# Optimization experiments

Hardware: AMD Instinct MI355X
Metric: run time of the kernel (lower is better)

## Reference

```python
import jax, jax.numpy as jnp
import numpy as np

D_MODEL = 1024
NHEAD = 16
D_K = D_MODEL // NHEAD


def setup_inputs() -> dict:
    key = jax.random.key(0)
    ks = jax.random.split(key, 8)
    B, S, D = 4, 2048, D_MODEL
    scale = 1.0 / np.sqrt(D)  # rough xavier-like scale for weights
    return {
        "query": jax.random.normal(ks[0], (B, S, D), jnp.float32),
        "key_": jax.random.normal(ks[1], (B, S, D), jnp.float32),
        "value": jax.random.normal(ks[2], (B, S, D), jnp.float32),
        "w_q": jax.random.normal(ks[3], (D, D), jnp.float32) * scale,
        "w_k": jax.random.normal(ks[4], (D, D), jnp.float32) * scale,
        "w_v": jax.random.normal(ks[5], (D, D), jnp.float32) * scale,
        "w_o": jax.random.normal(ks[6], (D, D), jnp.float32) * scale,
        "b_o": jnp.zeros((D,), jnp.float32),
    }


def reference(query, key_, value, w_q, w_k, w_v, w_o, b_o):
    B, S, D = query.shape
    H, dk = NHEAD, D_K
    # torch Linear: x @ W.T ; reshape to [B, H, S, dk]
    def split_heads(x, w):
        return (x @ w.T).reshape(B, S, H, dk).transpose(0, 2, 1, 3)

    Q = split_heads(query, w_q)
    K = split_heads(key_, w_k)
    V = split_heads(value, w_v)

    scores = jnp.einsum("bhqd,bhkd->bhqk", Q, K) / jnp.sqrt(jnp.float32(dk))
    attn = jax.nn.softmax(scores, axis=-1)  # [B,H,S,S]
    ctx = jnp.einsum("bhqk,bhkd->bhqd", attn, V)
    ctx = ctx.transpose(0, 2, 1, 3).reshape(B, S, D)
    out = ctx @ w_o.T + b_o
    return out
```

## Files before the change

kernel.cpp:

```cpp
#include <hip/hip_runtime.h>
#include <hip/hip_bf16.h>
#include <stdint.h>

#define D_MODEL 1024
#define NHEAD   16
#define DK      64
#define BATCH   4
#define SEQ     2048
#define MROWS   (BATCH*SEQ)

typedef __hip_bfloat16 bf16;
typedef __attribute__((ext_vector_type(8))) short short8;
typedef __attribute__((ext_vector_type(4))) float f32x4;
typedef __attribute__((ext_vector_type(4))) unsigned int uint4t;

typedef __attribute__((address_space(1))) unsigned int as1_uint;
typedef __attribute__((address_space(3))) unsigned int as3_uint;

#define MFMA32(a,b,c) __builtin_amdgcn_mfma_f32_16x16x32_bf16((a),(b),(c),0,0,0)

static __device__ __forceinline__ void load_lds16(const bf16* g, bf16* l) {
  __builtin_amdgcn_global_load_lds((const as1_uint*)g, (as3_uint*)l, 16, 0, 0);
}

static __device__ __forceinline__ unsigned short bfbits(float x) {
  __hip_bfloat16 h = __float2bfloat16(x);
  return __builtin_bit_cast(unsigned short, h);
}

static __device__ __forceinline__ unsigned int pack2(float lo, float hi) {
  return (unsigned int)bfbits(lo) | ((unsigned int)bfbits(hi) << 16);
}

static __device__ __forceinline__ unsigned int pack2t(float lo, float hi) {
  return (__builtin_bit_cast(unsigned int, lo) >> 16) |
         (__builtin_bit_cast(unsigned int, hi) & 0xffff0000u);
}

__global__ __launch_bounds__(256) void cast_w(const float* __restrict__ i0,
                                              const float* __restrict__ i1,
                                              const float* __restrict__ i2,
                                              const float* __restrict__ i3,
                                              bf16* o0, bf16* o1, bf16* o2, bf16* o3,
                                              float s1) {
  const int z = blockIdx.z;
  const float* in = z == 0 ? i0 : (z == 1 ? i1 : (z == 2 ? i2 : i3));
  bf16* out = z == 0 ? o0 : (z == 1 ? o1 : (z == 2 ? o2 : o3));
  const float s = (z == 1) ? s1 : 1.0f;
  int i = blockIdx.x * 256 + threadIdx.x;
  const float4* p = (const float4*)in;
  float4 a = p[2 * (size_t)i];
  float4 b = p[2 * (size_t)i + 1];
  uint4t u;
  u.x = pack2(a.x * s, a.y * s);
  u.y = pack2(a.z * s, a.w * s);
  u.z = pack2(b.x * s, b.y * s);
  u.w = pack2(b.z * s, b.w * s);
  *(uint4t*)(out + (size_t)i * 8) = u;
}

__global__ __launch_bounds__(256) void cast_x(const float* __restrict__ i0,
                                              const float* __restrict__ i1,
                                              const float* __restrict__ i2,
                                              bf16* o0, bf16* o1, bf16* o2) {
  const int z = blockIdx.z;
  const float* in = z == 0 ? i0 : (z == 1 ? i1 : i2);
  bf16* out = z == 0 ? o0 : (z == 1 ? o1 : o2);
  int i = blockIdx.x * 256 + threadIdx.x;
  const float4* p = (const float4*)in;
  float4 a = p[2 * (size_t)i];
  float4 b = p[2 * (size_t)i + 1];
  uint4t u;
  u.x = pack2(a.x, a.y);
  u.y = pack2(a.z, a.w);
  u.z = pack2(b.x, b.y);
  u.w = pack2(b.z, b.w);
  *(uint4t*)(out + (size_t)i * 8) = u;
}

__global__ __launch_bounds__(256) void gemm_proj(const bf16* __restrict__ A0,
                                                 const bf16* __restrict__ A1,
                                                 const bf16* __restrict__ A2,
                                                 const bf16* __restrict__ B0,
                                                 const bf16* __restrict__ B1,
                                                 const bf16* __restrict__ B2,
                                                 bf16* C0, bf16* C1, bf16* C2) {
  const int z = blockIdx.z;
  const bf16* A = z == 0 ? A0 : (z == 1 ? A1 : A2);
  const bf16* B = z == 0 ? B0 : (z == 1 ? B1 : B2);
  bf16* C = z == 0 ? C0 : (z == 1 ? C1 : C2);
  const int M = MROWS, N = D_MODEL, K = D_MODEL;

  __shared__ bf16 As[128 * 32];
  __shared__ bf16 Bs[128 * 32];
  const int t = threadIdx.x;
  const int w = t >> 6;
  const int lane = t & 63;
  const int lm = lane & 15;
  const int lq = lane >> 4;
  const int wm = (w >> 1) * 64;
  const int wn = (w & 1) * 64;
  const long rowA = (long)blockIdx.y * 128;
  const long rowB = (long)blockIdx.x * 128;

  const int srow = t >> 2;
  const int scol = (t & 3) * 8;
  const bf16* Ag0 = A + (rowA + srow) * K + scol;
  const bf16* Ag1 = A + (rowA + 64 + srow) * K + scol;
  const bf16* Bg0 = B + (rowB + srow) * K + scol;
  const bf16* Bg1 = B + (rowB + 64 + srow) * K + scol;
  bf16* As0 = As + w * 512;
  bf16* As1 = As + 2048 + w * 512;
  bf16* Bs0 = Bs + w * 512;
  bf16* Bs1 = Bs + 2048 + w * 512;

  const f32x4 fzero = {0.f, 0.f, 0.f, 0.f};
  f32x4 acc[4][4];
#pragma unroll
  for (int i = 0; i < 4; ++i)
#pragma unroll
    for (int j = 0; j < 4; ++j) acc[i][j] = fzero;

  for (int kt = 0; kt < K; kt += 32) {
    load_lds16(Ag0 + kt, As0);
    load_lds16(Ag1 + kt, As1);
    load_lds16(Bg0 + kt, Bs0);
    load_lds16(Bg1 + kt, Bs1);
    asm volatile("s_waitcnt vmcnt(0)" ::: "memory");
    __syncthreads();
    short8 af[4], bf_[4];
#pragma unroll
    for (int i = 0; i < 4; ++i) {
      af[i]  = *(const short8*)(As + (wm + i * 16 + lm) * 32 + lq * 8);
      bf_[i] = *(const short8*)(Bs + (wn + i * 16 + lm) * 32 + lq * 8);
    }
#pragma unroll
    for (int i = 0; i < 4; ++i)
#pragma unroll
      for (int j = 0; j < 4; ++j)
        acc[i][j] = MFMA32(af[i], bf_[j], acc[i][j]);
    __syncthreads();
  }

  if (z < 2) {
#pragma unroll
    for (int i = 0; i < 4; ++i) {
      long r0 = rowA + wm + i * 16 + lq * 4;
#pragma unroll
      for (int j = 0; j < 4; ++j) {
        long c = rowB + wn + j * 16 + lm;
#pragma unroll
        for (int r = 0; r < 4; ++r)
          C[(r0 + r) * N + c] = __float2bfloat16(acc[i][j][r]);
      }
    }
  } else {
#pragma unroll
    for (int j = 0; j < 4; ++j) {
      long c = rowB + wn + j * 16 + lm;
#pragma unroll
      for (int i = 0; i < 4; ++i) {
        long r0 = rowA + wm + i * 16 + lq * 4;
        long sp = (r0 & ~63L) | (((r0 >> 5) & 1) * 32) | ((r0 & 15) * 2) | ((r0 >> 4) & 1);
#pragma unroll
        for (int r = 0; r < 4; ++r)
          C[c * M + sp + r * 2] = __float2bfloat16(acc[i][j][r]);
      }
    }
  }
}

__global__ __launch_bounds__(256) void gemm_out(const bf16* __restrict__ A,
                                                const bf16* __restrict__ B,
                                                float* __restrict__ C,
                                                const float* __restrict__ bias) {
  const int M = MROWS, N = D_MODEL, K = D_MODEL;
  __shared__ bf16 As[128 * 32];
  __shared__ bf16 Bs[128 * 32];
  const int t = threadIdx.x;
  const int w = t >> 6;
  const int lane = t & 63;
  const int lm = lane & 15;
  const int lq = lane >> 4;
  const int wm = (w >> 1) * 64;
  const int wn = (w & 1) * 64;
  const long rowA = (long)blockIdx.y * 128;
  const long rowB = (long)blockIdx.x * 128;

  const int srow = t >> 2;
  const int scol = (t & 3) * 8;
  const bf16* Ag0 = A + (rowA + srow) * K + scol;
  const bf16* Ag1 = A + (rowA + 64 + srow) * K + scol;
  const bf16* Bg0 = B + (rowB + srow) * K + scol;
  const bf16* Bg1 = B + (rowB + 64 + srow) * K + scol;
  bf16* As0 = As + w * 512;
  bf16* As1 = As + 2048 + w * 512;
  bf16* Bs0 = Bs + w * 512;
  bf16* Bs1 = Bs + 2048 + w * 512;

  const f32x4 fzero = {0.f, 0.f, 0.f, 0.f};
  f32x4 acc[4][4];
#pragma unroll
  for (int i = 0; i < 4; ++i)
#pragma unroll
    for (int j = 0; j < 4; ++j) acc[i][j] = fzero;

  for (int kt = 0; kt < K; kt += 32) {
    load_lds16(Ag0 + kt, As0);
    load_lds16(Ag1 + kt, As1);
    load_lds16(Bg0 + kt, Bs0);
    load_lds16(Bg1 + kt, Bs1);
    asm volatile("s_waitcnt vmcnt(0)" ::: "memory");
    __syncthreads();
    short8 af[4], bf_[4];
#pragma unroll
    for (int i = 0; i < 4; ++i) {
      af[i]  = *(const short8*)(As + (wm + i * 16 + lm) * 32 + lq * 8);
      bf_[i] = *(const short8*)(Bs + (wn + i * 16 + lm) * 32 + lq * 8);
    }
#pragma unroll
    for (int i = 0; i < 4; ++i)
#pragma unroll
      for (int j = 0; j < 4; ++j)
        acc[i][j] = MFMA32(af[i], bf_[j], acc[i][j]);
    __syncthreads();
  }

#pragma unroll
  for (int j = 0; j < 4; ++j) {
    long c = rowB + wn + j * 16 + lm;
    float bz = bias[c];
#pragma unroll
    for (int i = 0; i < 4; ++i) {
      long r0 = rowA + wm + i * 16 + lq * 4;
#pragma unroll
      for (int r = 0; r < 4; ++r)
        C[(r0 + r) * N + c] = acc[i][j][r] + bz;
    }
  }
}

__global__ __launch_bounds__(256, 4) void attn_kernel(const bf16* __restrict__ Qb,
                                                      const bf16* __restrict__ Kb,
                                                      const bf16* __restrict__ Vt,
                                                      bf16* __restrict__ ctx) {
  __shared__ bf16 Ks[64 * 64];
  __shared__ bf16 Vs[64 * 64];
  const int t = threadIdx.x;
  const int w = t >> 6;
  const int lane = t & 63;
  const int lm = lane & 15;
  const int lq = lane >> 4;
  const int bh = blockIdx.x;
  const int b = bh >> 4;
  const int h = bh & 15;
  const int q0 = blockIdx.y * 128 + w * 32;

  const bf16* Qh = Qb + (long)b * SEQ * D_MODEL + h * DK;
  const bf16* Kh = Kb + (long)b * SEQ * D_MODEL + h * DK;
  const bf16* Vh = Vt + (long)h * DK * MROWS + (long)b * SEQ;

  const int sr = lane >> 3;
  const int sc = ((lane & 7) ^ sr) * 8;
  const bf16* kg0 = Kh + (long)(w * 8 + sr) * D_MODEL + sc;
  const bf16* kg1 = Kh + (long)(32 + w * 8 + sr) * D_MODEL + sc;
  const bf16* vg0 = Vh + (long)(w * 8 + sr) * MROWS + sc;
  const bf16* vg1 = Vh + (long)(32 + w * 8 + sr) * MROWS + sc;
  bf16* lk0 = Ks + w * 512;
  bf16* lk1 = Ks + 2048 + w * 512;
  bf16* lv0 = Vs + w * 512;
  bf16* lv1 = Vs + 2048 + w * 512;

  short8 qf[2][2];
#pragma unroll
  for (int qt = 0; qt < 2; ++qt)
#pragma unroll
    for (int ks = 0; ks < 2; ++ks)
      qf[qt][ks] = *(const short8*)(Qh + (long)(q0 + qt * 16 + lm) * D_MODEL + ks * 32 + lq * 8);

  uint4t uo;
  uo.x = 0x3F803F80u; uo.y = 0x3F803F80u; uo.z = 0x3F803F80u; uo.w = 0x3F803F80u;
  const short8 ones8 = __builtin_bit_cast(short8, uo);

  const f32x4 fzero = {0.f, 0.f, 0.f, 0.f};
  f32x4 O[2][4];
  f32x4 lsum[2];
#pragma unroll
  for (int qt = 0; qt < 2; ++qt) {
    lsum[qt] = fzero;
#pragma unroll
    for (int dt = 0; dt < 4; ++dt) O[qt][dt] = fzero;
  }

  const int xs = lm & 7;

  for (int kv = 0; kv < SEQ; kv += 64) {
    load_lds16(kg0, lk0);
    load_lds16(kg1, lk1);
    load_lds16(vg0, lv0);
    load_lds16(vg1, lv1);
    kg0 += 64 * D_MODEL; kg1 += 64 * D_MODEL;
    vg0 += 64; vg1 += 64;
    asm volatile("s_waitcnt vmcnt(0)" ::: "memory");
    __syncthreads();

    short8 kf[4][2];
#pragma unroll
    for (int c = 0; c < 4; ++c)
#pragma unroll
      for (int ks = 0; ks < 2; ++ks)
        kf[c][ks] = *(const short8*)(Ks + (c * 16 + lm) * 64 + (((ks * 4 + lq) ^ xs) * 8));
    short8 vf[4][2];
#pragma unroll
    for (int dt = 0; dt < 4; ++dt)
#pragma unroll
      for (int tt = 0; tt < 2; ++tt)
        vf[dt][tt] = *(const short8*)(Vs + (dt * 16 + lm) * 64 + (((tt * 4 + lq) ^ xs) * 8));

#pragma unroll
    for (int qt = 0; qt < 2; ++qt) {
      f32x4 st[4];
#pragma unroll
      for (int c = 0; c < 4; ++c)
        st[c] = MFMA32(kf[c][0], qf[qt][0], fzero);
#pragma unroll
      for (int c = 0; c < 4; ++c)
        st[c] = MFMA32(kf[c][1], qf[qt][1], st[c]);

      float pe[4][4];
#pragma unroll
      for (int c = 0; c < 4; ++c)
#pragma unroll
        for (int r = 0; r < 4; ++r)
          pe[c][r] = __builtin_amdgcn_exp2f(st[c][r]);

      short8 pf8[2];
#pragma unroll
      for (int tt = 0; tt < 2; ++tt) {
        uint4t u;
        u.x = pack2t(pe[2 * tt][0], pe[2 * tt + 1][0]);
        u.y = pack2t(pe[2 * tt][1], pe[2 * tt + 1][1]);
        u.z = pack2t(pe[2 * tt][2], pe[2 * tt + 1][2]);
        u.w = pack2t(pe[2 * tt][3], pe[2 * tt + 1][3]);
        pf8[tt] = __builtin_bit_cast(short8, u);
      }

#pragma unroll
      for (int tt = 0; tt < 2; ++tt) {
        lsum[qt] = MFMA32(pf8[tt], ones8, lsum[qt]);
#pragma unroll
        for (int dt = 0; dt < 4; ++dt)
          O[qt][dt] = MFMA32(pf8[tt], vf[dt][tt], O[qt][dt]);
      }
    }
    __syncthreads();
  }

#pragma unroll
  for (int qt = 0; qt < 2; ++qt) {
    f32x4 linv;
#pragma unroll
    for (int r = 0; r < 4; ++r) linv[r] = 1.f / lsum[qt][r];
#pragma unroll
    for (int r = 0; r < 4; ++r) {
      long qrow = (long)b * SEQ + q0 + qt * 16 + lq * 4 + r;
#pragma unroll
      for (int dt = 0; dt < 4; ++dt)
        ctx[qrow * D_MODEL + h * DK + dt * 16 + lm] =
            __float2bfloat16(O[qt][dt][r] * linv[r]);
    }
  }
}

extern "C" void kernel_launch(void* const* d_in, const int* in_sizes, int n_in,
                              void* d_out, int out_size, void* d_ws, size_t ws_size,
                              hipStream_t stream) {
  const float* q  = (const float*)d_in[0];
  const float* k  = (const float*)d_in[1];
  const float* v  = (const float*)d_in[2];
  const float* wq = (const float*)d_in[3];
  const float* wk = (const float*)d_in[4];
  const float* wv = (const float*)d_in[5];
  const float* wo = (const float*)d_in[6];
  const float* bo = (const float*)d_in[7];

  char* ws = (char*)d_ws;
  const size_t SZW = (size_t)D_MODEL * D_MODEL * sizeof(bf16);
  const size_t SZX = (size_t)MROWS * D_MODEL * sizeof(bf16);
  bf16* Wq = (bf16*)(ws + 0 * SZW);
  bf16* Wk = (bf16*)(ws + 1 * SZW);
  bf16* Wv = (bf16*)(ws + 2 * SZW);
  bf16* Wo = (bf16*)(ws + 3 * SZW);
  bf16* Xq = (bf16*)(ws + 4 * SZW + 0 * SZX);
  bf16* Xk = (bf16*)(ws + 4 * SZW + 1 * SZX);
  bf16* Xv = (bf16*)(ws + 4 * SZW + 2 * SZX);
  bf16* Qb = (bf16*)(ws + 4 * SZW + 3 * SZX);
  bf16* Kb = (bf16*)(ws + 4 * SZW + 4 * SZX);
  bf16* Vt = Xq;
  bf16* Cx = Xk;

  const float SCL = 0.18033688011112042f;
  const int NW8 = D_MODEL * D_MODEL / 8;
  const int NX8 = MROWS * D_MODEL / 8;

  cast_w<<<dim3(NW8 / 256, 1, 4), 256, 0, stream>>>(wq, wk, wv, wo, Wq, Wk, Wv, Wo, SCL);
  cast_x<<<dim3(NX8 / 256, 1, 3), 256, 0, stream>>>(q, k, v, Xq, Xk, Xv);

  gemm_proj<<<dim3(D_MODEL / 128, MROWS / 128, 3), 256, 0, stream>>>(
      Xq, Xk, Xv, Wq, Wk, Wv, Qb, Kb, Vt);

  attn_kernel<<<dim3(BATCH * NHEAD, SEQ / 128), 256, 0, stream>>>(Qb, Kb, Vt, Cx);

  gemm_out<<<dim3(D_MODEL / 128, MROWS / 128), 256, 0, stream>>>(Cx, Wo, (float*)d_out, bo);
}
```

Measured before the change: 332.4 us.

## Double-buffer LDS tiles in projection GEMMs and swap grid block ordering

Both GEMM kernels now use two LDS buffers and issue the global-to-LDS loads for the next k-slice before computing on the current one, overlapping memory latency with MFMA work and halving barriers per k-step. The grid dimensions are also swapped so consecutive blocks walk along M rows while sharing the same weight tile, changing cache locality. LDS use doubles per block, which may reduce occupancy.

```diff
diff --git a/kernel.cpp b/kernel.cpp
--- a/kernel.cpp
+++ b/kernel.cpp
@@ -78,6 +78,29 @@
   *(uint4t*)(out + (size_t)i * 8) = u;
 }
 
+#define GEMM_STAGE(BUFOFF, KT) do {                                   \
+    load_lds16(Ag0 + (KT), As + (BUFOFF) + w * 512);                  \
+    load_lds16(Ag1 + (KT), As + (BUFOFF) + 2048 + w * 512);           \
+    load_lds16(Bg0 + (KT), Bs + (BUFOFF) + w * 512);                  \
+    load_lds16(Bg1 + (KT), Bs + (BUFOFF) + 2048 + w * 512);           \
+  } while (0)
+
+#define GEMM_COMPUTE(BUFOFF) do {                                              \
+    short8 af[4], bf_[4];                                                      \
+    _Pragma("unroll") for (int i = 0; i < 4; ++i) {                            \
+      af[i]  = *(const short8*)(As + (BUFOFF) + (wm + i * 16 + lm) * 32 + lq * 8); \
+      bf_[i] = *(const short8*)(Bs + (BUFOFF) + (wn + i * 16 + lm) * 32 + lq * 8); \
+    }                                                                          \
+    _Pragma("unroll") for (int i = 0; i < 4; ++i)                              \
+      _Pragma("unroll") for (int j = 0; j < 4; ++j)                            \
+        acc[i][j] = MFMA32(af[i], bf_[j], acc[i][j]);                          \
+  } while (0)
+
+#define VMCNT0_BAR() do {                                   \
+    asm volatile("s_waitcnt vmcnt(0)" ::: "memory");        \
+    __syncthreads();                                        \
+  } while (0)
+
 __global__ __launch_bounds__(256) void gemm_proj(const bf16* __restrict__ A0,
                                                  const bf16* __restrict__ A1,
                                                  const bf16* __restrict__ A2,
@@ -91,8 +114,8 @@
   bf16* C = z == 0 ? C0 : (z == 1 ? C1 : C2);
   const int M = MROWS, N = D_MODEL, K = D_MODEL;
 
-  __shared__ bf16 As[128 * 32];
-  __shared__ bf16 Bs[128 * 32];
+  __shared__ bf16 As[2 * 128 * 32];
+  __shared__ bf16 Bs[2 * 128 * 32];
   const int t = threadIdx.x;
   const int w = t >> 6;
   const int lane = t & 63;
@@ -100,8 +123,8 @@
   const int lq = lane >> 4;
   const int wm = (w >> 1) * 64;
   const int wn = (w & 1) * 64;
-  const long rowA = (long)blockIdx.y * 128;
-  const long rowB = (long)blockIdx.x * 128;
+  const long rowA = (long)blockIdx.x * 128;
+  const long rowB = (long)blockIdx.y * 128;
 
   const int srow = t >> 2;
   const int scol = (t & 3) * 8;
@@ -109,10 +132,6 @@
   const bf16* Ag1 = A + (rowA + 64 + srow) * K + scol;
   const bf16* Bg0 = B + (rowB + srow) * K + scol;
   const bf16* Bg1 = B + (rowB + 64 + srow) * K + scol;
-  bf16* As0 = As + w * 512;
-  bf16* As1 = As + 2048 + w * 512;
-  bf16* Bs0 = Bs + w * 512;
-  bf16* Bs1 = Bs + 2048 + w * 512;
 
   const f32x4 fzero = {0.f, 0.f, 0.f, 0.f};
   f32x4 acc[4][4];
@@ -121,25 +140,15 @@
 #pragma unroll
     for (int j = 0; j < 4; ++j) acc[i][j] = fzero;
 
-  for (int kt = 0; kt < K; kt += 32) {
-    load_lds16(Ag0 + kt, As0);
-    load_lds16(Ag1 + kt, As1);
-    load_lds16(Bg0 + kt, Bs0);
-    load_lds16(Bg1 + kt, Bs1);
-    asm volatile("s_waitcnt vmcnt(0)" ::: "memory");
-    __syncthreads();
-    short8 af[4], bf_[4];
-#pragma unroll
-    for (int i = 0; i < 4; ++i) {
-      af[i]  = *(const short8*)(As + (wm + i * 16 + lm) * 32 + lq * 8);
-      bf_[i] = *(const short8*)(Bs + (wn + i * 16 + lm) * 32 + lq * 8);
-    }
-#pragma unroll
-    for (int i = 0; i < 4; ++i)
-#pragma unroll
-      for (int j = 0; j < 4; ++j)
-        acc[i][j] = MFMA32(af[i], bf_[j], acc[i][j]);
-    __syncthreads();
+  GEMM_STAGE(0, 0);
+  VMCNT0_BAR();
+  for (int kt = 0; kt < K; kt += 64) {
+    if (kt + 32 < K) GEMM_STAGE(4096, kt + 32);
+    GEMM_COMPUTE(0);
+    VMCNT0_BAR();
+    if (kt + 64 < K) GEMM_STAGE(0, kt + 64);
+    GEMM_COMPUTE(4096);
+    VMCNT0_BAR();
   }
 
   if (z < 2) {
@@ -175,8 +184,8 @@
                                                 float* __restrict__ C,
                                                 const float* __restrict__ bias) {
   const int M = MROWS, N = D_MODEL, K = D_MODEL;
-  __shared__ bf16 As[128 * 32];
-  __shared__ bf16 Bs[128 * 32];
+  __shared__ bf16 As[2 * 128 * 32];
+  __shared__ bf16 Bs[2 * 128 * 32];
   const int t = threadIdx.x;
   const int w = t >> 6;
   const int lane = t & 63;
@@ -184,8 +193,8 @@
   const int lq = lane >> 4;
   const int wm = (w >> 1) * 64;
   const int wn = (w & 1) * 64;
-  const long rowA = (long)blockIdx.y * 128;
-  const long rowB = (long)blockIdx.x * 128;
+  const long rowA = (long)blockIdx.x * 128;
+  const long rowB = (long)blockIdx.y * 128;
 
   const int srow = t >> 2;
   const int scol = (t & 3) * 8;
@@ -193,10 +202,6 @@
   const bf16* Ag1 = A + (rowA + 64 + srow) * K + scol;
   const bf16* Bg0 = B + (rowB + srow) * K + scol;
   const bf16* Bg1 = B + (rowB + 64 + srow) * K + scol;
-  bf16* As0 = As + w * 512;
-  bf16* As1 = As + 2048 + w * 512;
-  bf16* Bs0 = Bs + w * 512;
-  bf16* Bs1 = Bs + 2048 + w * 512;
 
   const f32x4 fzero = {0.f, 0.f, 0.f, 0.f};
   f32x4 acc[4][4];
@@ -205,25 +210,15 @@
 #pragma unroll
     for (int j = 0; j < 4; ++j) acc[i][j] = fzero;
 
-  for (int kt = 0; kt < K; kt += 32) {
-    load_lds16(Ag0 + kt, As0);
-    load_lds16(Ag1 + kt, As1);
-    load_lds16(Bg0 + kt, Bs0);
-    load_lds16(Bg1 + kt, Bs1);
-    asm volatile("s_waitcnt vmcnt(0)" ::: "memory");
-    __syncthreads();
-    short8 af[4], bf_[4];
-#pragma unroll
-    for (int i = 0; i < 4; ++i) {
-      af[i]  = *(const short8*)(As + (wm + i * 16 + lm) * 32 + lq * 8);
-      bf_[i] = *(const short8*)(Bs + (wn + i * 16 + lm) * 32 + lq * 8);
-    }
-#pragma unroll
-    for (int i = 0; i < 4; ++i)
-#pragma unroll
-      for (int j = 0; j < 4; ++j)
-        acc[i][j] = MFMA32(af[i], bf_[j], acc[i][j]);
-    __syncthreads();
+  GEMM_STAGE(0, 0);
+  VMCNT0_BAR();
+  for (int kt = 0; kt < K; kt += 64) {
+    if (kt + 32 < K) GEMM_STAGE(4096, kt + 32);
+    GEMM_COMPUTE(0);
+    VMCNT0_BAR();
+    if (kt + 64 < K) GEMM_STAGE(0, kt + 64);
+    GEMM_COMPUTE(4096);
+    VMCNT0_BAR();
   }
 
 #pragma unroll
@@ -406,10 +401,10 @@
   cast_w<<<dim3(NW8 / 256, 1, 4), 256, 0, stream>>>(wq, wk, wv, wo, Wq, Wk, Wv, Wo, SCL);
   cast_x<<<dim3(NX8 / 256, 1, 3), 256, 0, stream>>>(q, k, v, Xq, Xk, Xv);
 
-  gemm_proj<<<dim3(D_MODEL / 128, MROWS / 128, 3), 256, 0, stream>>>(
+  gemm_proj<<<dim3(MROWS / 128, D_MODEL / 128, 3), 256, 0, stream>>>(
       Xq, Xk, Xv, Wq, Wk, Wv, Qb, Kb, Vt);
 
   attn_kernel<<<dim3(BATCH * NHEAD, SEQ / 128), 256, 0, stream>>>(Qb, Kb, Vt, Cx);
 
-  gemm_out<<<dim3(D_MODEL / 128, MROWS / 128), 256, 0, stream>>>(Cx, Wo, (float*)d_out, bo);
-}
+  gemm_out<<<dim3(MROWS / 128, D_MODEL / 128), 256, 0, stream>>>(Cx, Wo, (float*)d_out, bo);
+}
```

New measurement: 326.4 us, median of 2. Within noise of the previous version (-1.8%).
